# Performance work log

Measured on AMD Instinct MI355X. Metric: run time of the kernel, lower is better.

The kernel has to match this reference:

```python
import jax, jax.numpy as jnp
import numpy as np

NUM_NODES = 50000
NUM_EDGES = 600000
IN_DIM = 128
OUT_DIM = 128


def setup_inputs() -> dict:
    key = jax.random.key(0)
    k1, k2, k3, k4, k5 = jax.random.split(key, 5)
    x = jax.random.normal(k1, (NUM_NODES, IN_DIM), dtype=jnp.float32)
    edge_index = jax.random.randint(k2, (2, NUM_EDGES), 0, NUM_NODES, dtype=jnp.int64)
    edge_weight = jax.random.uniform(k3, (NUM_EDGES,), dtype=jnp.float32)
    W = jax.random.normal(k4, (OUT_DIM, IN_DIM), dtype=jnp.float32) * (1.0 / np.sqrt(IN_DIM))
    b = jax.random.normal(k5, (OUT_DIM,), dtype=jnp.float32) * 0.01
    return {"x": x, "edge_index": edge_index, "edge_weight": edge_weight, "W": W, "b": b}


def reference(x, edge_index, edge_weight, W, b):
    num_nodes = x.shape[0]
    # add self loops
    loop = jnp.arange(num_nodes, dtype=edge_index.dtype)
    src = jnp.concatenate([edge_index[0], loop])           # [E + N]
    tgt = jnp.concatenate([edge_index[1], loop])           # [E + N]
    w = jnp.concatenate([edge_weight, jnp.ones((num_nodes,), dtype=edge_weight.dtype)])
    # degree via scatter-add over src, then symmetric normalization
    deg = jax.ops.segment_sum(w, src, num_segments=num_nodes)  # [N]
    dinv = 1.0 / jnp.sqrt(deg)
    w_norm = w * dinv[src] * dinv[tgt]                      # [E + N]
    # gather-scale-scatter aggregation
    msg = x[src] * w_norm[:, None]                          # [E + N, D]
    agg = jax.ops.segment_sum(msg, tgt, num_segments=num_nodes)  # [N, D]
    # dense linear (torch Linear convention)
    return agg @ W.T + b
```

## Files before the change

### kernel.cpp

```cpp
#include <hip/hip_runtime.h>

#define D 128
#define GROWS 32
#define RNG 13312
#define HCHUNKS 64


__device__ __forceinline__ unsigned bf16rne(float f) {
  unsigned u = __float_as_uint(f);
  return (u + 0x7FFFu + ((u >> 16) & 1u)) >> 16;
}

__device__ __forceinline__ float4 bf16x4(uint2 u) {
  float4 r;
  r.x = __uint_as_float(u.x << 16);
  r.y = __uint_as_float(u.x & 0xFFFF0000u);
  r.z = __uint_as_float(u.y << 16);
  r.w = __uint_as_float(u.y & 0xFFFF0000u);
  return r;
}

__global__ __launch_bounds__(256) void k_setup(const float* __restrict__ W,
                                               const int* __restrict__ ei,
                                               float* __restrict__ Wt,
                                               int* __restrict__ flag) {
  int i = blockIdx.x * 256 + threadIdx.x;
  if (i < D * D) {
    int c = i >> 7, k = i & 127;
    Wt[k * D + c] = W[i];
  }
  if (i == 0) {
    flag[0] = (ei[1] == 0 && ei[3] == 0 && ei[5] == 0 && ei[7] == 0) ? 1 : 0;
  }
}

__global__ __launch_bounds__(256) void k_gemm(const float* __restrict__ x,
                                              const float* __restrict__ Wt,
                                              uint2* __restrict__ yb,
                                              int N) {
  __shared__ float Xs[GROWS * D];
  const int tid = threadIdx.x;
  const int row0 = blockIdx.x * GROWS;

  for (int f = tid; f < GROWS * D / 4; f += 256) {
    int r = row0 + ((f * 4) >> 7);
    float4 v = make_float4(0.f, 0.f, 0.f, 0.f);
    if (r < N)
      v = reinterpret_cast<const float4*>(x)[(size_t)row0 * (D / 4) + f];
    reinterpret_cast<float4*>(Xs)[f] = v;
  }
  __syncthreads();

  const int c0 = (tid & 31) * 4;
  const int r0 = (tid >> 5) * 4;
  float acc[4][4];
#pragma unroll
  for (int i = 0; i < 4; ++i)
#pragma unroll
    for (int j = 0; j < 4; ++j) acc[i][j] = 0.f;

#pragma unroll 4
  for (int k = 0; k < D; ++k) {
    float4 wv = reinterpret_cast<const float4*>(Wt)[(k * D + c0) >> 2];
    float xr[4];
#pragma unroll
    for (int i = 0; i < 4; ++i) xr[i] = Xs[(r0 + i) * D + k];
#pragma unroll
    for (int i = 0; i < 4; ++i) {
      acc[i][0] += xr[i] * wv.x;
      acc[i][1] += xr[i] * wv.y;
      acc[i][2] += xr[i] * wv.z;
      acc[i][3] += xr[i] * wv.w;
    }
  }
#pragma unroll
  for (int i = 0; i < 4; ++i) {
    int row = row0 + r0 + i;
    if (row < N) {
      uint2 u;
      u.x = bf16rne(acc[i][0]) | (bf16rne(acc[i][1]) << 16);
      u.y = bf16rne(acc[i][2]) | (bf16rne(acc[i][3]) << 16);
      yb[(size_t)row * 32 + (tid & 31)] = u;
    }
  }
}

__global__ __launch_bounds__(256) void k_rank(const int* __restrict__ ei,
                                              int* __restrict__ cnt,
                                              int* __restrict__ rank,
                                              const int* __restrict__ flag,
                                              int E) {
  int e = blockIdx.x * 256 + threadIdx.x;
  if (e >= E) return;
  int t = flag[0] ? reinterpret_cast<const int2*>(ei)[E + e].x : ei[E + e];
  rank[e] = atomicAdd(&cnt[t], 1);
}

__global__ __launch_bounds__(256) void k_deghist(const int* __restrict__ ei,
                                                 const float* __restrict__ ew,
                                                 float* __restrict__ partial,
                                                 const int* __restrict__ flag,
                                                 int E) {
  __shared__ float h[RNG];
  const int tid = threadIdx.x;
  const int chunk = blockIdx.x, r = blockIdx.y;
  const int lo = r * RNG;
  for (int i = tid; i < RNG; i += 256) h[i] = 0.f;
  __syncthreads();

  const int epc = (E + HCHUNKS - 1) / HCHUNKS;
  const int e0 = chunk * epc;
  const int e1 = min(e0 + epc, E);
  const bool f64 = flag[0] != 0;
  for (int e = e0 + tid; e < e1; e += 256) {
    int s = f64 ? reinterpret_cast<const int2*>(ei)[e].x : ei[e];
    int d = s - lo;
    if ((unsigned)d < (unsigned)RNG) atomicAdd(&h[d], ew[e]);
  }
  __syncthreads();
  float* dst = partial + ((size_t)r * HCHUNKS + chunk) * RNG;
  for (int i = tid; i < RNG; i += 256) dst[i] = h[i];
}

__global__ __launch_bounds__(256) void k_degred(const float* __restrict__ partial,
                                                float* __restrict__ dinv,
                                                int N) {
  int i = blockIdx.x * 256 + threadIdx.x;
  if (i >= N) return;
  int r = i / RNG, off = i - r * RNG;
  const float* base = partial + (size_t)r * HCHUNKS * RNG + off;
  float s = 0.f;
#pragma unroll 8
  for (int c = 0; c < HCHUNKS; ++c) s += base[(size_t)c * RNG];
  dinv[i] = rsqrtf(s + 1.0f);
}

__device__ __forceinline__ int wave_incl_scan(int v, int lane) {
#pragma unroll
  for (int o = 1; o < 64; o <<= 1) {
    int t = __shfl_up(v, o);
    if (lane >= o) v += t;
  }
  return v;
}

__global__ __launch_bounds__(256) void k_scan1(const int* __restrict__ cnt,
                                               int* __restrict__ rowptr,
                                               int* __restrict__ blocksum,
                                               int N) {
  __shared__ int wtot[4];
  int tid = threadIdx.x;
  int i = blockIdx.x * 256 + tid;
  int v = (i < N) ? cnt[i] : 0;
  int lane = tid & 63, wv = tid >> 6;
  int inc = wave_incl_scan(v, lane);
  if (lane == 63) wtot[wv] = inc;
  __syncthreads();
  if (tid == 0) {
    int r = 0;
#pragma unroll
    for (int k = 0; k < 4; ++k) { int t = wtot[k]; wtot[k] = r; r += t; }
  }
  __syncthreads();
  int exc = wtot[wv] + inc - v;
  if (i < N) rowptr[i] = exc;
  if (tid == 255) blocksum[blockIdx.x] = wtot[3] + inc;
}

__global__ __launch_bounds__(64) void k_scan2(int* __restrict__ blocksum,
                                              int* __restrict__ blockoff,
                                              int nb) {
  int lane = threadIdx.x;
  int carry = 0;
  for (int base = 0; base < nb; base += 64) {
    int idx = base + lane;
    int v = (idx < nb) ? blocksum[idx] : 0;
    int inc = wave_incl_scan(v, lane);
    if (idx < nb) blockoff[idx] = carry + inc - v;
    carry += __shfl(inc, 63);
  }
}

__global__ __launch_bounds__(256) void k_scan3(int* __restrict__ rowptr,
                                               const int* __restrict__ blockoff,
                                               int N, int E) {
  int i = blockIdx.x * 256 + threadIdx.x;
  if (i < N) rowptr[i] += blockoff[blockIdx.x];
  if (i == 0) rowptr[N] = E;
}

__global__ __launch_bounds__(256) void k_scatter(const int* __restrict__ ei,
                                                 const float* __restrict__ w,
                                                 const float* __restrict__ dinv,
                                                 const int* __restrict__ rowptr,
                                                 const int* __restrict__ rank,
                                                 int2* __restrict__ edges,
                                                 const int* __restrict__ flag,
                                                 int E) {
  int e = blockIdx.x * 256 + threadIdx.x;
  if (e >= E) return;
  int s, t;
  if (flag[0]) {
    s = reinterpret_cast<const int2*>(ei)[e].x;
    t = reinterpret_cast<const int2*>(ei)[E + e].x;
  } else {
    s = ei[e];
    t = ei[E + e];
  }
  float wn = w[e] * dinv[s];
  edges[rowptr[t] + rank[e]] = make_int2(s, __float_as_int(wn));
}

__global__ __launch_bounds__(256) void k_gather(const int* __restrict__ rowptr,
                                                const int2* __restrict__ edges,
                                                const uint2* __restrict__ yb,
                                                const float* __restrict__ dinv,
                                                const float* __restrict__ b,
                                                float* __restrict__ out,
                                                int N) {
  const int tid = threadIdx.x;
  const int node = blockIdx.x * 4 + (tid >> 6);
  if (node >= N) return;
  const int lane = tid & 63, half = lane >> 5, l32 = lane & 31;

  const float dt = dinv[node];
  const float4 yself = bf16x4(yb[(size_t)node * 32 + l32]);
  const float4 bb = reinterpret_cast<const float4*>(b)[l32];

  float4 acc = make_float4(0.f, 0.f, 0.f, 0.f);
  const int end = rowptr[node + 1];
  int e = rowptr[node] + half;
  for (; e + 6 < end; e += 8) {
    int2 e0 = edges[e], e1 = edges[e + 2], e2 = edges[e + 4], e3 = edges[e + 6];
    float4 v0 = bf16x4(yb[(size_t)e0.x * 32 + l32]);
    float4 v1 = bf16x4(yb[(size_t)e1.x * 32 + l32]);
    float4 v2 = bf16x4(yb[(size_t)e2.x * 32 + l32]);
    float4 v3 = bf16x4(yb[(size_t)e3.x * 32 + l32]);
    float w0 = __int_as_float(e0.y), w1 = __int_as_float(e1.y);
    float w2 = __int_as_float(e2.y), w3 = __int_as_float(e3.y);
    acc.x += w0 * v0.x; acc.y += w0 * v0.y; acc.z += w0 * v0.z; acc.w += w0 * v0.w;
    acc.x += w1 * v1.x; acc.y += w1 * v1.y; acc.z += w1 * v1.z; acc.w += w1 * v1.w;
    acc.x += w2 * v2.x; acc.y += w2 * v2.y; acc.z += w2 * v2.z; acc.w += w2 * v2.w;
    acc.x += w3 * v3.x; acc.y += w3 * v3.y; acc.z += w3 * v3.z; acc.w += w3 * v3.w;
  }
  for (; e < end; e += 2) {
    int2 e0 = edges[e];
    float4 v0 = bf16x4(yb[(size_t)e0.x * 32 + l32]);
    float w0 = __int_as_float(e0.y);
    acc.x += w0 * v0.x; acc.y += w0 * v0.y; acc.z += w0 * v0.z; acc.w += w0 * v0.w;
  }
  acc.x += __shfl(acc.x, l32 + 32);
  acc.y += __shfl(acc.y, l32 + 32);
  acc.z += __shfl(acc.z, l32 + 32);
  acc.w += __shfl(acc.w, l32 + 32);
  if (half == 0) {
    float4 r;
    r.x = bb.x + dt * (acc.x + dt * yself.x);
    r.y = bb.y + dt * (acc.y + dt * yself.y);
    r.z = bb.z + dt * (acc.z + dt * yself.z);
    r.w = bb.w + dt * (acc.w + dt * yself.w);
    reinterpret_cast<float4*>(out)[(size_t)node * 32 + l32] = r;
  }
}

extern "C" void kernel_launch(void* const* d_in, const int* in_sizes, int n_in,
                              void* d_out, int out_size, void* d_ws, size_t ws_size,
                              hipStream_t stream) {
  const float* x = (const float*)d_in[0];
  const int* ei = (const int*)d_in[1];
  const float* ew = (const float*)d_in[2];
  const float* W = (const float*)d_in[3];
  const float* b = (const float*)d_in[4];
  float* out = (float*)d_out;

  const int N = in_sizes[0] / D;
  const int E = in_sizes[2];
  const int NB = (N + 255) / 256;
  const int nranges = (N + RNG - 1) / RNG;

  char* ws = (char*)d_ws;
  size_t off = 0;
  auto alloc = [&](size_t bytes) {
    char* p = ws + off;
    off = (off + bytes + 255) & ~(size_t)255;
    return p;
  };
  float* Wt = (float*)alloc((size_t)D * D * 4);
  uint2* yb = (uint2*)alloc((size_t)N * D * 2);
  float* dinv = (float*)alloc((size_t)N * 4);
  float* partial = (float*)alloc((size_t)nranges * HCHUNKS * RNG * 4);
  int* cnt = (int*)alloc((size_t)N * 4);
  int* rank = (int*)alloc((size_t)E * 4);
  int* rowptr = (int*)alloc((size_t)(N + 1) * 4);
  int* blocksum = (int*)alloc((size_t)NB * 4);
  int* blockoff = (int*)alloc((size_t)NB * 4);
  int2* edges = (int2*)alloc((size_t)E * 8);
  int* flag = (int*)alloc(4);

  hipMemsetAsync(cnt, 0, (size_t)N * 4, stream);
  hipLaunchKernelGGL(k_setup, dim3((D * D + 255) / 256), dim3(256), 0, stream,
                     W, ei, Wt, flag);
  hipLaunchKernelGGL(k_gemm, dim3((N + GROWS - 1) / GROWS), dim3(256), 0,
                     stream, x, Wt, yb, N);
  hipLaunchKernelGGL(k_deghist, dim3(HCHUNKS, nranges), dim3(256), 0, stream,
                     ei, ew, partial, flag, E);
  hipLaunchKernelGGL(k_degred, dim3(NB), dim3(256), 0, stream,
                     partial, dinv, N);
  hipLaunchKernelGGL(k_rank, dim3((E + 255) / 256), dim3(256), 0, stream,
                     ei, cnt, rank, flag, E);
  hipLaunchKernelGGL(k_scan1, dim3(NB), dim3(256), 0, stream,
                     cnt, rowptr, blocksum, N);
  hipLaunchKernelGGL(k_scan2, dim3(1), dim3(64), 0, stream,
                     blocksum, blockoff, NB);
  hipLaunchKernelGGL(k_scan3, dim3(NB), dim3(256), 0, stream,
                     rowptr, blockoff, N, E);
  hipLaunchKernelGGL(k_scatter, dim3((E + 255) / 256), dim3(256), 0, stream,
                     ei, ew, dinv, rowptr, rank, edges, flag, E);
  hipLaunchKernelGGL(k_gather, dim3((N + 3) / 4), dim3(256), 0, stream,
                     rowptr, edges, yb, dinv, b, out, N);
}
```

Before: 228.9 us.

## Build CSR with LDS-privatized count histograms and chunked scatter bases

Replaces the global-atomic rank counting with per-chunk shared-memory count histograms, fused into the degree histogram kernel. Per-chunk base offsets are derived in the scan phase, and the scatter uses shared-memory atomics to place edges. This removes global atomic contention, the rank array and the memset, and merges the degree reduction into the scan. The cost is extra partial-count traffic, a 64×N cbase array, and edge inputs read repeatedly across range blocks.

```diff
diff --git a/kernel.cpp b/kernel.cpp
--- a/kernel.cpp
+++ b/kernel.cpp
@@ -2,8 +2,9 @@
 
 #define D 128
 #define GROWS 32
-#define RNG 13312
 #define HCHUNKS 64
+#define RNG_H 8064
+#define RNG_S 16128
 
 
 __device__ __forceinline__ unsigned bf16rne(float f) {
@@ -85,54 +86,39 @@
   }
 }
 
-__global__ __launch_bounds__(256) void k_rank(const int* __restrict__ ei,
-                                              int* __restrict__ cnt,
-                                              int* __restrict__ rank,
+__global__ __launch_bounds__(256) void k_hist(const int* __restrict__ ei,
+                                              const float* __restrict__ ew,
+                                              float* __restrict__ pdeg,
+                                              int* __restrict__ pcnt,
                                               const int* __restrict__ flag,
                                               int E) {
-  int e = blockIdx.x * 256 + threadIdx.x;
-  if (e >= E) return;
-  int t = flag[0] ? reinterpret_cast<const int2*>(ei)[E + e].x : ei[E + e];
-  rank[e] = atomicAdd(&cnt[t], 1);
-}
-
-__global__ __launch_bounds__(256) void k_deghist(const int* __restrict__ ei,
-                                                 const float* __restrict__ ew,
-                                                 float* __restrict__ partial,
-                                                 const int* __restrict__ flag,
-                                                 int E) {
-  __shared__ float h[RNG];
+  __shared__ float hd[RNG_H];
+  __shared__ int hc[RNG_H];
   const int tid = threadIdx.x;
   const int chunk = blockIdx.x, r = blockIdx.y;
-  const int lo = r * RNG;
-  for (int i = tid; i < RNG; i += 256) h[i] = 0.f;
+  const int lo = r * RNG_H;
+  for (int i = tid; i < RNG_H; i += 256) { hd[i] = 0.f; hc[i] = 0; }
   __syncthreads();
 
   const int epc = (E + HCHUNKS - 1) / HCHUNKS;
   const int e0 = chunk * epc;
   const int e1 = min(e0 + epc, E);
   const bool f64 = flag[0] != 0;
+  const int2* ei2 = reinterpret_cast<const int2*>(ei);
   for (int e = e0 + tid; e < e1; e += 256) {
-    int s = f64 ? reinterpret_cast<const int2*>(ei)[e].x : ei[e];
-    int d = s - lo;
-    if ((unsigned)d < (unsigned)RNG) atomicAdd(&h[d], ew[e]);
-  }
-  __syncthreads();
-  float* dst = partial + ((size_t)r * HCHUNKS + chunk) * RNG;
-  for (int i = tid; i < RNG; i += 256) dst[i] = h[i];
-}
-
-__global__ __launch_bounds__(256) void k_degred(const float* __restrict__ partial,
-                                                float* __restrict__ dinv,
-                                                int N) {
-  int i = blockIdx.x * 256 + threadIdx.x;
-  if (i >= N) return;
-  int r = i / RNG, off = i - r * RNG;
-  const float* base = partial + (size_t)r * HCHUNKS * RNG + off;
-  float s = 0.f;
-#pragma unroll 8
-  for (int c = 0; c < HCHUNKS; ++c) s += base[(size_t)c * RNG];
-  dinv[i] = rsqrtf(s + 1.0f);
+    int s = f64 ? ei2[e].x : ei[e];
+    int t = f64 ? ei2[E + e].x : ei[E + e];
+    int ds = s - lo;
+    if ((unsigned)ds < (unsigned)RNG_H) atomicAdd(&hd[ds], ew[e]);
+    int dt = t - lo;
+    if ((unsigned)dt < (unsigned)RNG_H) atomicAdd(&hc[dt], 1);
+  }
+  __syncthreads();
+  size_t base = ((size_t)r * HCHUNKS + chunk) * RNG_H;
+  for (int i = tid; i < RNG_H; i += 256) {
+    pdeg[base + i] = hd[i];
+    pcnt[base + i] = hc[i];
+  }
 }
 
 __device__ __forceinline__ int wave_incl_scan(int v, int lane) {
@@ -144,14 +130,29 @@
   return v;
 }
 
-__global__ __launch_bounds__(256) void k_scan1(const int* __restrict__ cnt,
+__global__ __launch_bounds__(256) void k_scan1(const float* __restrict__ pdeg,
+                                               const int* __restrict__ pcnt,
+                                               float* __restrict__ dinv,
                                                int* __restrict__ rowptr,
                                                int* __restrict__ blocksum,
                                                int N) {
   __shared__ int wtot[4];
   int tid = threadIdx.x;
   int i = blockIdx.x * 256 + tid;
-  int v = (i < N) ? cnt[i] : 0;
+  int v = 0;
+  if (i < N) {
+    int r = i / RNG_H, off = i - r * RNG_H;
+    size_t base = (size_t)r * HCHUNKS * RNG_H + off;
+    float s = 0.f;
+    int c = 0;
+#pragma unroll 8
+    for (int k = 0; k < HCHUNKS; ++k) {
+      s += pdeg[base + (size_t)k * RNG_H];
+      c += pcnt[base + (size_t)k * RNG_H];
+    }
+    dinv[i] = rsqrtf(s + 1.0f);
+    v = c;
+  }
   int lane = tid & 63, wv = tid >> 6;
   int inc = wave_incl_scan(v, lane);
   if (lane == 63) wtot[wv] = inc;
@@ -181,34 +182,60 @@
   }
 }
 
-__global__ __launch_bounds__(256) void k_scan3(int* __restrict__ rowptr,
-                                               const int* __restrict__ blockoff,
-                                               int N, int E) {
+__global__ __launch_bounds__(256) void k_scan3base(int* __restrict__ rowptr,
+                                                   const int* __restrict__ blockoff,
+                                                   const int* __restrict__ pcnt,
+                                                   int* __restrict__ cbase,
+                                                   int N, int E) {
   int i = blockIdx.x * 256 + threadIdx.x;
-  if (i < N) rowptr[i] += blockoff[blockIdx.x];
+  if (i >= N) {
+    if (i == N) rowptr[N] = E;
+    return;
+  }
+  int rp = rowptr[i] + blockoff[blockIdx.x];
+  rowptr[i] = rp;
   if (i == 0) rowptr[N] = E;
+  int r = i / RNG_H, off = i - r * RNG_H;
+  size_t pb = (size_t)r * HCHUNKS * RNG_H + off;
+  int run = rp;
+#pragma unroll 8
+  for (int c = 0; c < HCHUNKS; ++c) {
+    cbase[(size_t)c * N + i] = run;
+    run += pcnt[pb + (size_t)c * RNG_H];
+  }
 }
 
 __global__ __launch_bounds__(256) void k_scatter(const int* __restrict__ ei,
-                                                 const float* __restrict__ w,
+                                                 const float* __restrict__ ew,
                                                  const float* __restrict__ dinv,
-                                                 const int* __restrict__ rowptr,
-                                                 const int* __restrict__ rank,
+                                                 const int* __restrict__ cbase,
                                                  int2* __restrict__ edges,
                                                  const int* __restrict__ flag,
-                                                 int E) {
-  int e = blockIdx.x * 256 + threadIdx.x;
-  if (e >= E) return;
-  int s, t;
-  if (flag[0]) {
-    s = reinterpret_cast<const int2*>(ei)[e].x;
-    t = reinterpret_cast<const int2*>(ei)[E + e].x;
-  } else {
-    s = ei[e];
-    t = ei[E + e];
-  }
-  float wn = w[e] * dinv[s];
-  edges[rowptr[t] + rank[e]] = make_int2(s, __float_as_int(wn));
+                                                 int N, int E) {
+  __shared__ int hb[RNG_S];
+  const int tid = threadIdx.x;
+  const int chunk = blockIdx.x, r = blockIdx.y;
+  const int lo = r * RNG_S;
+  for (int j = tid; j < RNG_S; j += 256) {
+    int v = lo + j;
+    hb[j] = (v < N) ? cbase[(size_t)chunk * N + v] : 0;
+  }
+  __syncthreads();
+
+  const int epc = (E + HCHUNKS - 1) / HCHUNKS;
+  const int e0 = chunk * epc;
+  const int e1 = min(e0 + epc, E);
+  const bool f64 = flag[0] != 0;
+  const int2* ei2 = reinterpret_cast<const int2*>(ei);
+  for (int e = e0 + tid; e < e1; e += 256) {
+    int t = f64 ? ei2[E + e].x : ei[E + e];
+    int dt = t - lo;
+    if ((unsigned)dt < (unsigned)RNG_S) {
+      int s = f64 ? ei2[e].x : ei[e];
+      int pos = atomicAdd(&hb[dt], 1);
+      edges[pos] = make_int2(s, __float_as_int(ew[e] * dinv[s]));
+    }
+  }
 }
 
 __global__ __launch_bounds__(256) void k_gather(const int* __restrict__ rowptr,
@@ -276,7 +303,8 @@
   const int N = in_sizes[0] / D;
   const int E = in_sizes[2];
   const int NB = (N + 255) / 256;
-  const int nranges = (N + RNG - 1) / RNG;
+  const int nrH = (N + RNG_H - 1) / RNG_H;
+  const int nrS = (N + RNG_S - 1) / RNG_S;
 
   char* ws = (char*)d_ws;
   size_t off = 0;
@@ -288,34 +316,29 @@
   float* Wt = (float*)alloc((size_t)D * D * 4);
   uint2* yb = (uint2*)alloc((size_t)N * D * 2);
   float* dinv = (float*)alloc((size_t)N * 4);
-  float* partial = (float*)alloc((size_t)nranges * HCHUNKS * RNG * 4);
-  int* cnt = (int*)alloc((size_t)N * 4);
-  int* rank = (int*)alloc((size_t)E * 4);
+  float* pdeg = (float*)alloc((size_t)nrH * HCHUNKS * RNG_H * 4);
+  int* pcnt = (int*)alloc((size_t)nrH * HCHUNKS * RNG_H * 4);
+  int* cbase = (int*)alloc((size_t)HCHUNKS * N * 4);
   int* rowptr = (int*)alloc((size_t)(N + 1) * 4);
   int* blocksum = (int*)alloc((size_t)NB * 4);
   int* blockoff = (int*)alloc((size_t)NB * 4);
   int2* edges = (int2*)alloc((size_t)E * 8);
   int* flag = (int*)alloc(4);
 
-  hipMemsetAsync(cnt, 0, (size_t)N * 4, stream);
   hipLaunchKernelGGL(k_setup, dim3((D * D + 255) / 256), dim3(256), 0, stream,
                      W, ei, Wt, flag);
   hipLaunchKernelGGL(k_gemm, dim3((N + GROWS - 1) / GROWS), dim3(256), 0,
                      stream, x, Wt, yb, N);
-  hipLaunchKernelGGL(k_deghist, dim3(HCHUNKS, nranges), dim3(256), 0, stream,
-                     ei, ew, partial, flag, E);
-  hipLaunchKernelGGL(k_degred, dim3(NB), dim3(256), 0, stream,
-                     partial, dinv, N);
-  hipLaunchKernelGGL(k_rank, dim3((E + 255) / 256), dim3(256), 0, stream,
-                     ei, cnt, rank, flag, E);
+  hipLaunchKernelGGL(k_hist, dim3(HCHUNKS, nrH), dim3(256), 0, stream,
+                     ei, ew, pdeg, pcnt, flag, E);
   hipLaunchKernelGGL(k_scan1, dim3(NB), dim3(256), 0, stream,
-                     cnt, rowptr, blocksum, N);
+                     pdeg, pcnt, dinv, rowptr, blocksum, N);
   hipLaunchKernelGGL(k_scan2, dim3(1), dim3(64), 0, stream,
                      blocksum, blockoff, NB);
-  hipLaunchKernelGGL(k_scan3, dim3(NB), dim3(256), 0, stream,
-                     rowptr, blockoff, N, E);
-  hipLaunchKernelGGL(k_scatter, dim3((E + 255) / 256), dim3(256), 0, stream,
-                     ei, ew, dinv, rowptr, rank, edges, flag, E);
+  hipLaunchKernelGGL(k_scan3base, dim3(NB), dim3(256), 0, stream,
+                     rowptr, blockoff, pcnt, cbase, N, E);
+  hipLaunchKernelGGL(k_scatter, dim3(HCHUNKS, nrS), dim3(256), 0, stream,
+                     ei, ew, dinv, cbase, edges, flag, N, E);
   hipLaunchKernelGGL(k_gather, dim3((N + 3) / 4), dim3(256), 0, stream,
                      rowptr, edges, yb, dinv, b, out, N);
 }
```

Measured after the change: 229.8 us. No clear change (+0.4%).
